# Kernel optimization log

Hardware: AMD Instinct MI355X
Metric: run time of the kernel (lower is better)

## Reference

```python
import jax, jax.numpy as jnp
import numpy as np

N = 100000   # total nodes across all graphs
E = 1600000  # directed edges
G = 2048     # number of graphs in the batch
F_IN = 10    # len(ATOM_TYPES)
LATENT = 64


def setup_inputs() -> dict:
    key = jax.random.key(0)
    ks = jax.random.split(key, 13)

    def lin_w(k, fi, fo):
        return (jax.random.normal(k, (fi, fo), dtype=jnp.float32) / np.sqrt(fi)).astype(jnp.float32)

    return {
        "x": jax.random.normal(ks[0], (N, F_IN), dtype=jnp.float32),
        "edge_index": jax.random.randint(ks[1], (2, E), 0, N),
        "batch": jnp.sort(jax.random.randint(ks[2], (N,), 0, G)),
        "W1": lin_w(ks[3], F_IN, 128), "b1": 0.01 * jax.random.normal(ks[4], (128,), dtype=jnp.float32),
        "W2": lin_w(ks[5], 128, 256), "b2": 0.01 * jax.random.normal(ks[6], (256,), dtype=jnp.float32),
        "W3": lin_w(ks[7], 256, 256), "b3": 0.01 * jax.random.normal(ks[8], (256,), dtype=jnp.float32),
        "Wmu": lin_w(ks[9], 256, LATENT), "bmu": 0.01 * jax.random.normal(ks[10], (LATENT,), dtype=jnp.float32),
        "Wlv": lin_w(ks[11], 256, LATENT), "blv": 0.01 * jax.random.normal(ks[12], (LATENT,), dtype=jnp.float32),
    }


def reference(x, edge_index, batch, W1, b1, W2, b2, W3, b3, Wmu, bmu, Wlv, blv):
    n = x.shape[0]
    # GCNConv: add self-loops, symmetric degree normalization (PyG semantics)
    loop = jnp.arange(n)
    src = jnp.concatenate([edge_index[0], loop])  # message source j
    dst = jnp.concatenate([edge_index[1], loop])  # aggregation target i
    deg = jax.ops.segment_sum(jnp.ones(src.shape[0], x.dtype), dst, num_segments=n)
    dis = jnp.where(deg > 0, jax.lax.rsqrt(jnp.maximum(deg, 1e-12)), 0.0)
    norm = (dis[src] * dis[dst])[:, None]  # [E+N, 1]

    def gcn(h, W, b):
        h = h @ W                                   # transform first (cheaper gather)
        msg = h[src] * norm                         # gather + scale
        return jax.ops.segment_sum(msg, dst, num_segments=n) + b  # scatter-add

    h = jax.nn.relu(gcn(x, W1, b1))
    h = jax.nn.relu(gcn(h, W2, b2))
    h = jax.nn.relu(gcn(h, W3, b3))

    # global_mean_pool over graph ids
    sums = jax.ops.segment_sum(h, batch, num_segments=G)               # [G, 256]
    cnt = jax.ops.segment_sum(jnp.ones((n,), h.dtype), batch, num_segments=G)
    pooled = sums / jnp.maximum(cnt, 1.0)[:, None]

    return (pooled @ Wmu + bmu, pooled @ Wlv + blv)
```

## Files before the change

### kernel.cpp

```cpp
#include <hip/hip_runtime.h>
#include <hip/hip_bf16.h>
#include <math.h>


#define THREADS 256
#define SCAN_CHUNK 4096

typedef __attribute__((ext_vector_type(8))) short bf16x8;
typedef __attribute__((ext_vector_type(4))) float f32x4;

__global__ void setup_kernel(int* deg,
                             const float* __restrict__ W2, __hip_bfloat16* __restrict__ W2T,
                             const float* __restrict__ W3, __hip_bfloat16* __restrict__ W3T,
                             const int* __restrict__ batch, int* goff,
                             int n, int g) {
    int i = blockIdx.x * blockDim.x + threadIdx.x;
    if (i < n) deg[i] = 1;
    int r2 = i - n;
    if (r2 >= 0 && r2 < 128 * 256) {
        int k = r2 >> 8, c = r2 & 255;
        W2T[c * 128 + k] = __float2bfloat16(W2[r2]);
    }
    int r3 = i - n - 128 * 256;
    if (r3 >= 0 && r3 < 256 * 256) {
        int k = r3 >> 8, c = r3 & 255;
        W3T[c * 256 + k] = __float2bfloat16(W3[r3]);
    }
    int r4 = i - n - 128 * 256 - 256 * 256;
    if (r4 >= 0 && r4 < n) {
        int j = r4;
        int b = batch[j];
        if (j == 0) {
            for (int q = 0; q <= b; ++q) goff[q] = 0;
        } else {
            int bp = batch[j - 1];
            for (int q = bp + 1; q <= b; ++q) goff[q] = j;
        }
        if (j == n - 1) {
            for (int q = b + 1; q <= g; ++q) goff[q] = n;
        }
    }
}

__global__ __launch_bounds__(THREADS) void hist_deg_kernel(
        const int* __restrict__ dst, int* deg, int e, int n) {
    const int slice = blockIdx.x & 7;
    const int sliceSize = (n + 7) / 8;
    const int lo = slice * sliceSize;
    const int hi = lo + sliceSize;
    const int tid = (blockIdx.x >> 3) * blockDim.x + threadIdx.x;
    const int nthr = (gridDim.x >> 3) * blockDim.x;
    const int e4 = e >> 2;
    const uint4* dst4 = reinterpret_cast<const uint4*>(dst);
    for (int i = tid; i < e4; i += nthr) {
        uint4 dv = dst4[i];
        int dd[4] = {(int)dv.x, (int)dv.y, (int)dv.z, (int)dv.w};
#pragma unroll
        for (int q = 0; q < 4; ++q)
            if (dd[q] >= lo && dd[q] < hi) atomicAdd(&deg[dd[q]], 1);
    }
    for (int i = (e & ~3) + tid; i < e; i += nthr) {
        int d = dst[i];
        if (d >= lo && d < hi) atomicAdd(&deg[d], 1);
    }
}

__global__ __launch_bounds__(1024) void scan_part_kernel(
        const int* __restrict__ deg, int* __restrict__ bsum, int n) {
    __shared__ int ws[16];
    const int lane = threadIdx.x & 63;
    const int wid = threadIdx.x >> 6;
    int i0 = blockIdx.x * SCAN_CHUNK + threadIdx.x * 4;
    int s = 0;
#pragma unroll
    for (int q = 0; q < 4; ++q) {
        int i = i0 + q;
        if (i < n) s += deg[i] - 1;
    }
#pragma unroll
    for (int off = 32; off > 0; off >>= 1) s += __shfl_down(s, off, 64);
    if (lane == 0) ws[wid] = s;
    __syncthreads();
    if (threadIdx.x == 0) {
        int t = 0;
        for (int w = 0; w < 16; ++w) t += ws[w];
        bsum[blockIdx.x] = t;
    }
}

__device__ __forceinline__ unsigned pack2(float a, float b) {
    unsigned short ua = __builtin_bit_cast(unsigned short, __float2bfloat16(a));
    unsigned short ub = __builtin_bit_cast(unsigned short, __float2bfloat16(b));
    return (unsigned)ua | ((unsigned)ub << 16);
}

__global__ __launch_bounds__(1024) void scan_final_kernel(
        const int* __restrict__ deg, const int* __restrict__ bsum, int nb,
        int* __restrict__ row_ptr, int* __restrict__ cursor,
        float* __restrict__ dis, const float* __restrict__ x,
        __hip_bfloat16* __restrict__ xd, int n) {
    __shared__ int wsum[16];
    __shared__ int sbase;
    const int lane = threadIdx.x & 63;
    const int wid = threadIdx.x >> 6;
    if (threadIdx.x == 0) {
        int t = 0;
        for (int b = 0; b < blockIdx.x; ++b) t += bsum[b];
        sbase = t;
        if (blockIdx.x == 0) {
            int tot = 0;
            for (int b = 0; b < nb; ++b) tot += bsum[b];
            row_ptr[n] = tot;
        }
    }
    int i0 = blockIdx.x * SCAN_CHUNK + threadIdx.x * 4;
    int v[4];
#pragma unroll
    for (int q = 0; q < 4; ++q) {
        int i = i0 + q;
        v[q] = (i < n) ? (deg[i] - 1) : 0;
    }
    int tsum = v[0] + v[1] + v[2] + v[3];
    int incl = tsum;
#pragma unroll
    for (int off = 1; off < 64; off <<= 1) {
        int t = __shfl_up(incl, off, 64);
        if (lane >= off) incl += t;
    }
    if (lane == 63) wsum[wid] = incl;
    __syncthreads();
    int wbase = 0;
    for (int w = 0; w < wid; ++w) wbase += wsum[w];
    int pos = incl - tsum + wbase + sbase;
    uint4* xd4 = reinterpret_cast<uint4*>(xd);
#pragma unroll
    for (int q = 0; q < 4; ++q) {
        int i = i0 + q;
        if (i < n) {
            row_ptr[i] = pos;
            cursor[i] = pos;
            float dv = rsqrtf((float)(v[q] + 1));
            dis[i] = dv;
            unsigned ow[8];
#pragma unroll
            for (int k = 0; k < 5; ++k)
                ow[k] = pack2(x[(size_t)i * 10 + 2 * k] * dv,
                              x[(size_t)i * 10 + 2 * k + 1] * dv);
            ow[5] = 0; ow[6] = 0; ow[7] = 0;
            xd4[(size_t)i * 2]     = make_uint4(ow[0], ow[1], ow[2], ow[3]);
            xd4[(size_t)i * 2 + 1] = make_uint4(ow[4], ow[5], ow[6], ow[7]);
        }
        pos += v[q];
    }
}

__global__ __launch_bounds__(THREADS) void fill_csr_kernel(
        const int* __restrict__ src, const int* __restrict__ dst,
        int* cursor, int* __restrict__ col, int e, int n) {
    const int slice = blockIdx.x & 7;
    const int sliceSize = (n + 7) / 8;
    const int lo = slice * sliceSize;
    const int hi = lo + sliceSize;
    const int tid = (blockIdx.x >> 3) * blockDim.x + threadIdx.x;
    const int nthr = (gridDim.x >> 3) * blockDim.x;
    const int e4 = e >> 2;
    const uint4* dst4 = reinterpret_cast<const uint4*>(dst);
    const uint4* src4 = reinterpret_cast<const uint4*>(src);
    for (int i = tid; i < e4; i += nthr) {
        uint4 dv = dst4[i];
        int dd[4] = {(int)dv.x, (int)dv.y, (int)dv.z, (int)dv.w};
        bool any = false;
#pragma unroll
        for (int q = 0; q < 4; ++q) any |= (dd[q] >= lo && dd[q] < hi);
        if (!any) continue;
        uint4 sv = src4[i];
        int ss[4] = {(int)sv.x, (int)sv.y, (int)sv.z, (int)sv.w};
#pragma unroll
        for (int q = 0; q < 4; ++q) {
            if (dd[q] >= lo && dd[q] < hi) {
                int pos = atomicAdd(&cursor[dd[q]], 1);
                col[pos] = ss[q];
            }
        }
    }
    for (int i = (e & ~3) + tid; i < e; i += nthr) {
        int d = dst[i];
        if (d >= lo && d < hi) {
            int pos = atomicAdd(&cursor[d], 1);
            col[pos] = src[i];
        }
    }
}

__device__ __forceinline__ void acc8(float* acc, uint4 v) {
    acc[0] += __uint_as_float(v.x << 16);
    acc[1] += __uint_as_float(v.x & 0xffff0000u);
    acc[2] += __uint_as_float(v.y << 16);
    acc[3] += __uint_as_float(v.y & 0xffff0000u);
    acc[4] += __uint_as_float(v.z << 16);
    acc[5] += __uint_as_float(v.z & 0xffff0000u);
    acc[6] += __uint_as_float(v.w << 16);
    acc[7] += __uint_as_float(v.w & 0xffff0000u);
}

__global__ __launch_bounds__(THREADS) void layer1_kernel(
        const __hip_bfloat16* __restrict__ xd, const int* __restrict__ row_ptr,
        const int* __restrict__ col, const float* __restrict__ dis,
        const float* __restrict__ W1, const float* __restrict__ b1,
        __hip_bfloat16* __restrict__ out, int n) {
    __shared__ float h[128][12];
    __shared__ float w[10][128];
    __shared__ float bias[128];

    for (int idx = threadIdx.x; idx < 1280; idx += THREADS)
        w[idx >> 7][idx & 127] = W1[idx];
    if (threadIdx.x < 128) bias[threadIdx.x] = b1[threadIdx.x];

    const int node0 = blockIdx.x * 128;
    const int nl = threadIdx.x >> 1;
    const int lane = threadIdx.x & 1;
    const int node = node0 + nl;
    const uint4* S4 = reinterpret_cast<const uint4*>(xd);

    if (node < n) {
        float acc[8];
#pragma unroll
        for (int q = 0; q < 8; ++q) acc[q] = 0.f;
        acc8(acc, S4[(size_t)node * 2 + lane]);

        int s = row_ptr[node], e = row_ptr[node + 1];
        int p = s;
        for (; p + 8 <= e; p += 8) {
            int j[8];
#pragma unroll
            for (int q = 0; q < 8; ++q) j[q] = col[p + q];
            uint4 v[8];
#pragma unroll
            for (int q = 0; q < 8; ++q) v[q] = S4[(size_t)j[q] * 2 + lane];
#pragma unroll
            for (int q = 0; q < 8; ++q) acc8(acc, v[q]);
        }
        for (; p < e; ++p) acc8(acc, S4[(size_t)col[p] * 2 + lane]);

        float dn = dis[node];
        if (lane == 0) {
#pragma unroll
            for (int q = 0; q < 8; ++q) h[nl][q] = acc[q] * dn;
        } else {
            h[nl][8] = acc[0] * dn;
            h[nl][9] = acc[1] * dn;
        }
    }
    __syncthreads();

    const int half = threadIdx.x & 1;
    const int nodeB = node0 + (threadIdx.x >> 1);
    if (nodeB < n) {
        float dnB = dis[nodeB];
        float hv[10];
#pragma unroll
        for (int k = 0; k < 10; ++k) hv[k] = h[threadIdx.x >> 1][k];
#pragma unroll
        for (int step = 0; step < 8; ++step) {
            int c0 = half * 64 + step * 8;
            unsigned rr[4];
#pragma unroll
            for (int cc = 0; cc < 8; cc += 2) {
                float a0 = bias[c0 + cc], a1 = bias[c0 + cc + 1];
#pragma unroll
                for (int k = 0; k < 10; ++k) {
                    a0 = fmaf(hv[k], w[k][c0 + cc], a0);
                    a1 = fmaf(hv[k], w[k][c0 + cc + 1], a1);
                }
                rr[cc >> 1] = pack2(fmaxf(a0, 0.f) * dnB, fmaxf(a1, 0.f) * dnB);
            }
            reinterpret_cast<uint4*>(out)[((size_t)nodeB * 128 + c0) >> 3] =
                make_uint4(rr[0], rr[1], rr[2], rr[3]);
        }
    }
}

template <int COLS, int L>
__global__ __launch_bounds__(THREADS) void agg_bf16_kernel(
        const __hip_bfloat16* __restrict__ S, const int* __restrict__ row_ptr,
        const int* __restrict__ col, const float* __restrict__ dis,
        __hip_bfloat16* __restrict__ out, int n) {
    static_assert(L * 8 == COLS, "");
    constexpr int stride = COLS / 8;
    int node = blockIdx.x * (THREADS / L) + threadIdx.x / L;
    if (node >= n) return;
    int lane = threadIdx.x % L;
    const uint4* S4 = reinterpret_cast<const uint4*>(S);

    float acc[8];
#pragma unroll
    for (int q = 0; q < 8; ++q) acc[q] = 0.f;
    acc8(acc, S4[(size_t)node * stride + lane]);

    int s = row_ptr[node], e = row_ptr[node + 1];
    int p = s;
    for (; p + 8 <= e; p += 8) {
        int j[8];
#pragma unroll
        for (int q = 0; q < 8; ++q) j[q] = col[p + q];
        uint4 v[8];
#pragma unroll
        for (int q = 0; q < 8; ++q) v[q] = S4[(size_t)j[q] * stride + lane];
#pragma unroll
        for (int q = 0; q < 8; ++q) acc8(acc, v[q]);
    }
    for (; p + 2 <= e; p += 2) {
        int j0 = col[p], j1 = col[p + 1];
        uint4 v0 = S4[(size_t)j0 * stride + lane];
        uint4 v1 = S4[(size_t)j1 * stride + lane];
        acc8(acc, v0); acc8(acc, v1);
    }
    for (; p < e; ++p) acc8(acc, S4[(size_t)col[p] * stride + lane]);

    float d = dis[node];
    uint4 o;
    o.x = pack2(acc[0] * d, acc[1] * d);
    o.y = pack2(acc[2] * d, acc[3] * d);
    o.z = pack2(acc[4] * d, acc[5] * d);
    o.w = pack2(acc[6] * d, acc[7] * d);
    reinterpret_cast<uint4*>(out)[(size_t)node * stride + lane] = o;
}

template <int K, bool SCALE>
__global__ __launch_bounds__(THREADS) void transform_mfma2_kernel(
        const __hip_bfloat16* __restrict__ A, const __hip_bfloat16* __restrict__ WT,
        const float* __restrict__ b, const float* __restrict__ dis,
        __hip_bfloat16* __restrict__ out, int n, int ntiles) {
    constexpr int KS = K / 32;
    constexpr int TSTR = 264;
    __shared__ __hip_bfloat16 tile[16 * TSTR];
    const int wave = threadIdx.x >> 6;
    const int lane = threadIdx.x & 63;
    const int lrow = lane & 15;
    const int lk8  = (lane >> 4) * 8;

    const uint4* WT4 = reinterpret_cast<const uint4*>(WT);
    bf16x8 bfr[4][KS];
    float bias[4];
#pragma unroll
    for (int ct = 0; ct < 4; ++ct) {
        int colc = wave * 64 + ct * 16 + lrow;
        bias[ct] = b[colc];
#pragma unroll
        for (int kk = 0; kk < KS; ++kk)
            bfr[ct][kk] = __builtin_bit_cast(
                bf16x8, WT4[((size_t)colc * K + kk * 32 + lk8) >> 3]);
    }

    const uint4* A4 = reinterpret_cast<const uint4*>(A);
    auto loadA = [&](int t, uint4* av) {
        int row = t * 16 + lrow;
        if (row >= n) row = n - 1;
#pragma unroll
        for (int kk = 0; kk < KS; ++kk)
            av[kk] = A4[((size_t)row * K + kk * 32 + lk8) >> 3];
    };

    uint4 aC[KS], aN[KS];
    int t = blockIdx.x;
    if (t < ntiles) loadA(t, aC);

    for (; t < ntiles; t += gridDim.x) {
        int tn = t + gridDim.x;
        if (tn < ntiles) loadA(tn, aN);

        f32x4 acc[4];
#pragma unroll
        for (int ct = 0; ct < 4; ++ct) acc[ct] = (f32x4){0.f, 0.f, 0.f, 0.f};
#pragma unroll
        for (int kk = 0; kk < KS; ++kk) {
            bf16x8 af = __builtin_bit_cast(bf16x8, aC[kk]);
#pragma unroll
            for (int ct = 0; ct < 4; ++ct)
                acc[ct] = __builtin_amdgcn_mfma_f32_16x16x32_bf16(af, bfr[ct][kk], acc[ct], 0, 0, 0);
        }

        const int lrow0 = (lane >> 4) * 4;
        float dv[4];
#pragma unroll
        for (int r = 0; r < 4; ++r) {
            int rr = t * 16 + lrow0 + r;
            dv[r] = SCALE ? ((rr < n) ? dis[rr] : 0.f) : 1.f;
        }
#pragma unroll
        for (int ct = 0; ct < 4; ++ct) {
            int colc = wave * 64 + ct * 16 + lrow;
#pragma unroll
            for (int r = 0; r < 4; ++r) {
                float v = fmaxf(acc[ct][r] + bias[ct], 0.f);
                if (SCALE) v *= dv[r];
                tile[(lrow0 + r) * TSTR + colc] = __float2bfloat16(v);
            }
        }
        __syncthreads();

        const int base = t * 16;
        if (base + 16 <= n) {
            uint4* g = reinterpret_cast<uint4*>(out + (size_t)base * 256);
            const uint4* tl = reinterpret_cast<const uint4*>(tile);
#pragma unroll
            for (int h = 0; h < 2; ++h) {
                int idx = threadIdx.x + h * 256;
                int row = idx >> 5, c16 = idx & 31;
                g[idx] = tl[row * (TSTR / 8) + c16];
            }
        } else {
            for (int idx = threadIdx.x; idx < 16 * 256; idx += THREADS) {
                int rr = base + (idx >> 8);
                if (rr < n) out[(size_t)rr * 256 + (idx & 255)] = tile[(idx >> 8) * TSTR + (idx & 255)];
            }
        }
        __syncthreads();

#pragma unroll
        for (int kk = 0; kk < KS; ++kk) aC[kk] = aN[kk];
    }
}

__global__ __launch_bounds__(THREADS) void pool_heads_kernel(
        const __hip_bfloat16* __restrict__ H, const int* __restrict__ goff,
        const float* __restrict__ Wmu, const float* __restrict__ bmu,
        const float* __restrict__ Wlv, const float* __restrict__ blv,
        float* __restrict__ out, int g_total) {
    __shared__ float part[8][256];
    __shared__ float p[256];
    int g = blockIdx.x;
    int s = goff[g], e = goff[g + 1];
    int rgrp = threadIdx.x >> 5;
    int lane = threadIdx.x & 31;
    const uint4* H4 = reinterpret_cast<const uint4*>(H);

    float acc[8];
#pragma unroll
    for (int q = 0; q < 8; ++q) acc[q] = 0.f;
    for (int r = s + rgrp; r < e; r += 8)
        acc8(acc, H4[(size_t)r * 32 + lane]);
#pragma unroll
    for (int q = 0; q < 8; ++q) part[rgrp][lane * 8 + q] = acc[q];
    __syncthreads();

    int c = threadIdx.x;
    float t = 0.f;
#pragma unroll
    for (int gq = 0; gq < 8; ++gq) t += part[gq][c];
    p[c] = t / fmaxf((float)(e - s), 1.0f);
    __syncthreads();

    if (threadIdx.x < 128) {
        int cc = threadIdx.x & 63;
        bool is_mu = threadIdx.x < 64;
        const float* W = is_mu ? Wmu : Wlv;
        const float* bb = is_mu ? bmu : blv;
        float a = 0.f;
        for (int k = 0; k < 256; ++k) a = fmaf(p[k], W[k * 64 + cc], a);
        float* o = is_mu ? (out + (size_t)g * 64)
                         : (out + (size_t)g_total * 64 + (size_t)g * 64);
        o[cc] = a + bb[cc];
    }
}

extern "C" void kernel_launch(void* const* d_in, const int* in_sizes, int n_in,
                              void* d_out, int out_size, void* d_ws, size_t ws_size,
                              hipStream_t stream) {
    const float* x      = (const float*)d_in[0];
    const int*   eidx   = (const int*)d_in[1];
    const int*   batch  = (const int*)d_in[2];
    const float* W1  = (const float*)d_in[3];
    const float* b1  = (const float*)d_in[4];
    const float* W2  = (const float*)d_in[5];
    const float* b2  = (const float*)d_in[6];
    const float* W3  = (const float*)d_in[7];
    const float* b3  = (const float*)d_in[8];
    const float* Wmu = (const float*)d_in[9];
    const float* bmu = (const float*)d_in[10];
    const float* Wlv = (const float*)d_in[11];
    const float* blv = (const float*)d_in[12];
    float* out = (float*)d_out;

    const int N = in_sizes[0] / 10;
    const int E = in_sizes[1] / 2;
    const int G = out_size / 128;

    const int* src = eidx;
    const int* dst = eidx + E;

    __hip_bfloat16* SA = (__hip_bfloat16*)d_ws;
    __hip_bfloat16* SB = SA + (size_t)N * 256;
    float* dis  = (float*)(SB + (size_t)N * 256);
    __hip_bfloat16* W2T = (__hip_bfloat16*)(dis + N);
    __hip_bfloat16* W3T = W2T + 256 * 128;
    __hip_bfloat16* xd  = W3T + 256 * 256;
    int* deg     = (int*)(xd + (size_t)N * 16);
    int* row_ptr = deg + N;
    int* cursor  = row_ptr + N + 1;
    int* col     = cursor + N;
    int* goff    = col + E;
    int* bsum    = goff + G + 1;

    const int ntiles = (N + 15) / 16;
    const int nb = (N + SCAN_CHUNK - 1) / SCAN_CHUNK;

    {
        int total = 2 * N + 128 * 256 + 256 * 256;
        setup_kernel<<<(total + THREADS - 1) / THREADS, THREADS, 0, stream>>>(
            deg, W2, W2T, W3, W3T, batch, goff, N, G);
    }
    hist_deg_kernel<<<2048, THREADS, 0, stream>>>(dst, deg, E, N);
    scan_part_kernel<<<nb, 1024, 0, stream>>>(deg, bsum, N);
    scan_final_kernel<<<nb, 1024, 0, stream>>>(deg, bsum, nb, row_ptr, cursor, dis, x, xd, N);
    fill_csr_kernel<<<2048, THREADS, 0, stream>>>(src, dst, cursor, col, E, N);

    layer1_kernel<<<(N + 127) / 128, THREADS, 0, stream>>>(
        xd, row_ptr, col, dis, W1, b1, SA, N);

    agg_bf16_kernel<128, 16><<<(N + 15) / 16, THREADS, 0, stream>>>(SA, row_ptr, col, dis, SB, N);
    transform_mfma2_kernel<128, true><<<512, THREADS, 0, stream>>>(SB, W2T, b2, dis, SA, N, ntiles);

    agg_bf16_kernel<256, 32><<<(N + 7) / 8, THREADS, 0, stream>>>(SA, row_ptr, col, dis, SB, N);
    transform_mfma2_kernel<256, false><<<512, THREADS, 0, stream>>>(SB, W3T, b3, dis, SA, N, ntiles);

    pool_heads_kernel<<<G, THREADS, 0, stream>>>(SA, goff, Wmu, bmu, Wlv, blv, out, G);
}
```

Baseline: 456.8 us.

## Fuse CSR aggregation with MFMA transform into one per-layer kernel

Merges the gather/aggregate kernel and the MFMA dense transform for layers 2 and 3 into one persistent kernel. Each block aggregates 16 nodes into a swizzled LDS tile and then multiplies it by the register-resident weight fragments, so the aggregated intermediate no longer makes a round trip through global memory and two launches are dropped. In exchange, the gather phase and the MFMA phase are serialized within each block with extra barriers. The cross-tile prefetch of A is removed, and occupancy is limited to 1024 persistent blocks with launch_bounds of 2.

```diff
diff --git a/kernel.cpp b/kernel.cpp
--- a/kernel.cpp
+++ b/kernel.cpp
@@ -280,60 +280,20 @@
     }
 }
 
-template <int COLS, int L>
-__global__ __launch_bounds__(THREADS) void agg_bf16_kernel(
+template <int K, bool SCALE>
+__global__ __launch_bounds__(THREADS, 2) void fused_layer_kernel(
         const __hip_bfloat16* __restrict__ S, const int* __restrict__ row_ptr,
         const int* __restrict__ col, const float* __restrict__ dis,
-        __hip_bfloat16* __restrict__ out, int n) {
-    static_assert(L * 8 == COLS, "");
-    constexpr int stride = COLS / 8;
-    int node = blockIdx.x * (THREADS / L) + threadIdx.x / L;
-    if (node >= n) return;
-    int lane = threadIdx.x % L;
-    const uint4* S4 = reinterpret_cast<const uint4*>(S);
-
-    float acc[8];
-#pragma unroll
-    for (int q = 0; q < 8; ++q) acc[q] = 0.f;
-    acc8(acc, S4[(size_t)node * stride + lane]);
-
-    int s = row_ptr[node], e = row_ptr[node + 1];
-    int p = s;
-    for (; p + 8 <= e; p += 8) {
-        int j[8];
-#pragma unroll
-        for (int q = 0; q < 8; ++q) j[q] = col[p + q];
-        uint4 v[8];
-#pragma unroll
-        for (int q = 0; q < 8; ++q) v[q] = S4[(size_t)j[q] * stride + lane];
-#pragma unroll
-        for (int q = 0; q < 8; ++q) acc8(acc, v[q]);
-    }
-    for (; p + 2 <= e; p += 2) {
-        int j0 = col[p], j1 = col[p + 1];
-        uint4 v0 = S4[(size_t)j0 * stride + lane];
-        uint4 v1 = S4[(size_t)j1 * stride + lane];
-        acc8(acc, v0); acc8(acc, v1);
-    }
-    for (; p < e; ++p) acc8(acc, S4[(size_t)col[p] * stride + lane]);
-
-    float d = dis[node];
-    uint4 o;
-    o.x = pack2(acc[0] * d, acc[1] * d);
-    o.y = pack2(acc[2] * d, acc[3] * d);
-    o.z = pack2(acc[4] * d, acc[5] * d);
-    o.w = pack2(acc[6] * d, acc[7] * d);
-    reinterpret_cast<uint4*>(out)[(size_t)node * stride + lane] = o;
-}
-
-template <int K, bool SCALE>
-__global__ __launch_bounds__(THREADS) void transform_mfma2_kernel(
-        const __hip_bfloat16* __restrict__ A, const __hip_bfloat16* __restrict__ WT,
-        const float* __restrict__ b, const float* __restrict__ dis,
+        const __hip_bfloat16* __restrict__ WT, const float* __restrict__ b,
         __hip_bfloat16* __restrict__ out, int n, int ntiles) {
     constexpr int KS = K / 32;
+    constexpr int L = K / 8;
+    constexpr int NPB = THREADS / L;
+    constexpr int PASSES = 16 / NPB;
     constexpr int TSTR = 264;
-    __shared__ __hip_bfloat16 tile[16 * TSTR];
+    __shared__ uint4 atile[16 * L];
+    __shared__ __hip_bfloat16 otile[16 * TSTR];
+
     const int wave = threadIdx.x >> 6;
     const int lane = threadIdx.x & 63;
     const int lrow = lane & 15;
@@ -352,29 +312,60 @@
                 bf16x8, WT4[((size_t)colc * K + kk * 32 + lk8) >> 3]);
     }
 
-    const uint4* A4 = reinterpret_cast<const uint4*>(A);
-    auto loadA = [&](int t, uint4* av) {
-        int row = t * 16 + lrow;
-        if (row >= n) row = n - 1;
-#pragma unroll
-        for (int kk = 0; kk < KS; ++kk)
-            av[kk] = A4[((size_t)row * K + kk * 32 + lk8) >> 3];
-    };
-
-    uint4 aC[KS], aN[KS];
-    int t = blockIdx.x;
-    if (t < ntiles) loadA(t, aC);
-
-    for (; t < ntiles; t += gridDim.x) {
-        int tn = t + gridDim.x;
-        if (tn < ntiles) loadA(tn, aN);
+    const uint4* S4 = reinterpret_cast<const uint4*>(S);
+    const int gn = threadIdx.x / L;
+    const int gl = threadIdx.x % L;
+
+    for (int t = blockIdx.x; t < ntiles; t += gridDim.x) {
+#pragma unroll
+        for (int ps = 0; ps < PASSES; ++ps) {
+            int nl = ps * NPB + gn;
+            int node = t * 16 + nl;
+            uint4 o = make_uint4(0, 0, 0, 0);
+            if (node < n) {
+                float acc[8];
+#pragma unroll
+                for (int q = 0; q < 8; ++q) acc[q] = 0.f;
+                acc8(acc, S4[(size_t)node * L + gl]);
+
+                int s = row_ptr[node], e = row_ptr[node + 1];
+                int p = s;
+                for (; p + 8 <= e; p += 8) {
+                    int j[8];
+#pragma unroll
+                    for (int q = 0; q < 8; ++q) j[q] = col[p + q];
+                    uint4 v[8];
+#pragma unroll
+                    for (int q = 0; q < 8; ++q) v[q] = S4[(size_t)j[q] * L + gl];
+#pragma unroll
+                    for (int q = 0; q < 8; ++q) acc8(acc, v[q]);
+                }
+                for (; p + 2 <= e; p += 2) {
+                    int j0 = col[p], j1 = col[p + 1];
+                    uint4 v0 = S4[(size_t)j0 * L + gl];
+                    uint4 v1 = S4[(size_t)j1 * L + gl];
+                    acc8(acc, v0); acc8(acc, v1);
+                }
+                for (; p < e; ++p) acc8(acc, S4[(size_t)col[p] * L + gl]);
+
+                float d = dis[node];
+                o.x = pack2(acc[0] * d, acc[1] * d);
+                o.y = pack2(acc[2] * d, acc[3] * d);
+                o.z = pack2(acc[4] * d, acc[5] * d);
+                o.w = pack2(acc[6] * d, acc[7] * d);
+            }
+            atile[nl * L + (gl ^ (nl & 7))] = o;
+        }
+        __syncthreads();
 
         f32x4 acc[4];
 #pragma unroll
         for (int ct = 0; ct < 4; ++ct) acc[ct] = (f32x4){0.f, 0.f, 0.f, 0.f};
 #pragma unroll
         for (int kk = 0; kk < KS; ++kk) {
-            bf16x8 af = __builtin_bit_cast(bf16x8, aC[kk]);
+            int chunk = kk * 4 + (lk8 >> 3);
+            uint4 av = atile[lrow * L + (chunk ^ (lrow & 7))];
+            bf16x8 af = __builtin_bit_cast(bf16x8, av);
 #pragma unroll
             for (int ct = 0; ct < 4; ++ct)
                 acc[ct] = __builtin_amdgcn_mfma_f32_16x16x32_bf16(af, bfr[ct][kk], acc[ct], 0, 0, 0);
@@ -394,7 +385,7 @@
             for (int r = 0; r < 4; ++r) {
                 float v = fmaxf(acc[ct][r] + bias[ct], 0.f);
                 if (SCALE) v *= dv[r];
-                tile[(lrow0 + r) * TSTR + colc] = __float2bfloat16(v);
+                otile[(lrow0 + r) * TSTR + colc] = __float2bfloat16(v);
             }
         }
         __syncthreads();
@@ -402,23 +393,22 @@
         const int base = t * 16;
         if (base + 16 <= n) {
             uint4* g = reinterpret_cast<uint4*>(out + (size_t)base * 256);
-            const uint4* tl = reinterpret_cast<const uint4*>(tile);
-#pragma unroll
-            for (int h = 0; h < 2; ++h) {
-                int idx = threadIdx.x + h * 256;
+            const uint4* tl = reinterpret_cast<const uint4*>(otile);
+#pragma unroll
+            for (int hh = 0; hh < 2; ++hh) {
+                int idx = threadIdx.x + hh * 256;
                 int row = idx >> 5, c16 = idx & 31;
                 g[idx] = tl[row * (TSTR / 8) + c16];
             }
         } else {
             for (int idx = threadIdx.x; idx < 16 * 256; idx += THREADS) {
                 int rr = base + (idx >> 8);
-                if (rr < n) out[(size_t)rr * 256 + (idx & 255)] = tile[(idx >> 8) * TSTR + (idx & 255)];
+                if (rr < n)
+                    out[(size_t)rr * 256 + (idx & 255)] =
+                        otile[(idx >> 8) * TSTR + (idx & 255)];
             }
         }
         __syncthreads();
-
-#pragma unroll
-        for (int kk = 0; kk < KS; ++kk) aC[kk] = aN[kk];
     }
 }
 
@@ -518,11 +508,11 @@
     layer1_kernel<<<(N + 127) / 128, THREADS, 0, stream>>>(
         xd, row_ptr, col, dis, W1, b1, SA, N);
 
-    agg_bf16_kernel<128, 16><<<(N + 15) / 16, THREADS, 0, stream>>>(SA, row_ptr, col, dis, SB, N);
-    transform_mfma2_kernel<128, true><<<512, THREADS, 0, stream>>>(SB, W2T, b2, dis, SA, N, ntiles);
-
-    agg_bf16_kernel<256, 32><<<(N + 7) / 8, THREADS, 0, stream>>>(SA, row_ptr, col, dis, SB, N);
-    transform_mfma2_kernel<256, false><<<512, THREADS, 0, stream>>>(SB, W3T, b3, dis, SA, N, ntiles);
+    fused_layer_kernel<128, true><<<1024, THREADS, 0, stream>>>(
+        SA, row_ptr, col, dis, W2T, b2, SB, N, ntiles);
+
+    fused_layer_kernel<256, false><<<1024, THREADS, 0, stream>>>(
+        SB, row_ptr, col, dis, W3T, b3, SA, N, ntiles);
 
     pool_heads_kernel<<<G, THREADS, 0, stream>>>(SA, goff, Wmu, bmu, Wlv, blv, out, G);
 }
```

New measurement: 470.6 us. 1.03x slower.

## Fuse layer-2 neighbor aggregation with MFMA transform in one persistent kernel

Applied to the files above, without the earlier changes.

Replaces the separate layer-2 aggregation kernel and MFMA transform kernel with a single persistent kernel. Each block gathers the neighbor sums for 16 nodes into a swizzled shared-memory tile, then multiplies that tile by W2 with MFMA. Bias, ReLU and the degree scaling are applied in the same pass and the result is written out. This removes the global-memory round trip of the aggregated 128-wide intermediate and one launch. The cost is extra syncs and lower occupancy, since gather latency now shares the same blocks as the MFMA work. Buffer roles for later stages are swapped to match.

```diff
diff --git a/kernel.cpp b/kernel.cpp
--- a/kernel.cpp
+++ b/kernel.cpp
@@ -326,6 +326,130 @@
     reinterpret_cast<uint4*>(out)[(size_t)node * stride + lane] = o;
 }
 
+__global__ __launch_bounds__(THREADS, 3) void fused128_kernel(
+        const __hip_bfloat16* __restrict__ S, const int* __restrict__ row_ptr,
+        const int* __restrict__ col, const float* __restrict__ dis,
+        const __hip_bfloat16* __restrict__ WT, const float* __restrict__ b,
+        __hip_bfloat16* __restrict__ out, int n, int ntiles) {
+    constexpr int K = 128, KS = 4, L = 16, TSTR = 264;
+    __shared__ uint4 atile[16 * L];
+    __shared__ __hip_bfloat16 otile[16 * TSTR];
+
+    const int wave = threadIdx.x >> 6;
+    const int lane = threadIdx.x & 63;
+    const int lrow = lane & 15;
+    const int lk8  = (lane >> 4) * 8;
+
+    const uint4* WT4 = reinterpret_cast<const uint4*>(WT);
+    bf16x8 bfr[4][KS];
+    float bias[4];
+#pragma unroll
+    for (int ct = 0; ct < 4; ++ct) {
+        int colc = wave * 64 + ct * 16 + lrow;
+        bias[ct] = b[colc];
+#pragma unroll
+        for (int kk = 0; kk < KS; ++kk)
+            bfr[ct][kk] = __builtin_bit_cast(
+                bf16x8, WT4[((size_t)colc * K + kk * 32 + lk8) >> 3]);
+    }
+
+    const uint4* S4 = reinterpret_cast<const uint4*>(S);
+    const int gn = threadIdx.x / L;
+    const int gl = threadIdx.x % L;
+
+    for (int t = blockIdx.x; t < ntiles; t += gridDim.x) {
+        {
+            int node = t * 16 + gn;
+            uint4 o = make_uint4(0, 0, 0, 0);
+            if (node < n) {
+                float acc[8];
+#pragma unroll
+                for (int q = 0; q < 8; ++q) acc[q] = 0.f;
+                acc8(acc, S4[(size_t)node * L + gl]);
+
+                int s = row_ptr[node], e = row_ptr[node + 1];
+                int p = s;
+                for (; p + 8 <= e; p += 8) {
+                    int j[8];
+#pragma unroll
+                    for (int q = 0; q < 8; ++q) j[q] = col[p + q];
+                    uint4 v[8];
+#pragma unroll
+                    for (int q = 0; q < 8; ++q) v[q] = S4[(size_t)j[q] * L + gl];
+#pragma unroll
+                    for (int q = 0; q < 8; ++q) acc8(acc, v[q]);
+                }
+                for (; p + 2 <= e; p += 2) {
+                    int j0 = col[p], j1 = col[p + 1];
+                    uint4 v0 = S4[(size_t)j0 * L + gl];
+                    uint4 v1 = S4[(size_t)j1 * L + gl];
+                    acc8(acc, v0); acc8(acc, v1);
+                }
+                for (; p < e; ++p) acc8(acc, S4[(size_t)col[p] * L + gl]);
+
+                float d = dis[node];
+                o.x = pack2(acc[0] * d, acc[1] * d);
+                o.y = pack2(acc[2] * d, acc[3] * d);
+                o.z = pack2(acc[4] * d, acc[5] * d);
+                o.w = pack2(acc[6] * d, acc[7] * d);
+            }
+            atile[gn * L + (gl ^ (gn & 7))] = o;
+        }
+        __syncthreads();
+
+        f32x4 acc[4];
+#pragma unroll
+        for (int ct = 0; ct < 4; ++ct) acc[ct] = (f32x4){0.f, 0.f, 0.f, 0.f};
+#pragma unroll
+        for (int kk = 0; kk < KS; ++kk) {
+            int chunk = kk * 4 + (lk8 >> 3);
+            uint4 av = atile[lrow * L + (chunk ^ (lrow & 7))];
+            bf16x8 af = __builtin_bit_cast(bf16x8, av);
+#pragma unroll
+            for (int ct = 0; ct < 4; ++ct)
+                acc[ct] = __builtin_amdgcn_mfma_f32_16x16x32_bf16(af, bfr[ct][kk], acc[ct], 0, 0, 0);
+        }
+
+        const int lrow0 = (lane >> 4) * 4;
+        float dv[4];
+#pragma unroll
+        for (int r = 0; r < 4; ++r) {
+            int rr = t * 16 + lrow0 + r;
+            dv[r] = (rr < n) ? dis[rr] : 0.f;
+        }
+#pragma unroll
+        for (int ct = 0; ct < 4; ++ct) {
+            int colc = wave * 64 + ct * 16 + lrow;
+#pragma unroll
+            for (int r = 0; r < 4; ++r) {
+                float v = fmaxf(acc[ct][r] + bias[ct], 0.f) * dv[r];
+                otile[(lrow0 + r) * TSTR + colc] = __float2bfloat16(v);
+            }
+        }
+        __syncthreads();
+
+        const int base = t * 16;
+        if (base + 16 <= n) {
+            uint4* g = reinterpret_cast<uint4*>(out + (size_t)base * 256);
+            const uint4* tl = reinterpret_cast<const uint4*>(otile);
+#pragma unroll
+            for (int hh = 0; hh < 2; ++hh) {
+                int idx = threadIdx.x + hh * 256;
+                int row = idx >> 5, c16 = idx & 31;
+                g[idx] = tl[row * (TSTR / 8) + c16];
+            }
+        } else {
+            for (int idx = threadIdx.x; idx < 16 * 256; idx += THREADS) {
+                int rr = base + (idx >> 8);
+                if (rr < n)
+                    out[(size_t)rr * 256 + (idx & 255)] =
+                        otile[(idx >> 8) * TSTR + (idx & 255)];
+            }
+        }
+        __syncthreads();
+    }
+}
+
 template <int K, bool SCALE>
 __global__ __launch_bounds__(THREADS) void transform_mfma2_kernel(
         const __hip_bfloat16* __restrict__ A, const __hip_bfloat16* __restrict__ WT,
@@ -518,11 +642,11 @@
     layer1_kernel<<<(N + 127) / 128, THREADS, 0, stream>>>(
         xd, row_ptr, col, dis, W1, b1, SA, N);
 
-    agg_bf16_kernel<128, 16><<<(N + 15) / 16, THREADS, 0, stream>>>(SA, row_ptr, col, dis, SB, N);
-    transform_mfma2_kernel<128, true><<<512, THREADS, 0, stream>>>(SB, W2T, b2, dis, SA, N, ntiles);
-
-    agg_bf16_kernel<256, 32><<<(N + 7) / 8, THREADS, 0, stream>>>(SA, row_ptr, col, dis, SB, N);
-    transform_mfma2_kernel<256, false><<<512, THREADS, 0, stream>>>(SB, W3T, b3, dis, SA, N, ntiles);
-
-    pool_heads_kernel<<<G, THREADS, 0, stream>>>(SA, goff, Wmu, bmu, Wlv, blv, out, G);
-}
+    fused128_kernel<<<2048, THREADS, 0, stream>>>(
+        SA, row_ptr, col, dis, W2T, b2, SB, N, ntiles);
+
+    agg_bf16_kernel<256, 32><<<(N + 7) / 8, THREADS, 0, stream>>>(SB, row_ptr, col, dis, SA, N);
+    transform_mfma2_kernel<256, false><<<512, THREADS, 0, stream>>>(SA, W3T, b3, dis, SB, N, ntiles);
+
+    pool_heads_kernel<<<G, THREADS, 0, stream>>>(SB, goff, Wmu, bmu, Wlv, blv, out, G);
+}
```

After: 454.9 us. No clear change (-0.4%).
